# Performance work log

Measured on AMD Instinct MI355X. Metric: run time of the kernel, lower is better.

Reference implementation:

```python
import jax, jax.numpy as jnp
import numpy as np
import math

P = 2
TAU = 1.0
USE_POW = False
ALIGN_W = 1.0
ENTROPY_W = 1.0
EPS = 1e-12


def _pairwise_l2(z):
    # torch.cdist(z, z, p=2): sqrt of squared distances via GEMM decomposition
    sq = jnp.sum(z * z, axis=-1)  # [N]
    d2 = sq[:, None] + sq[None, :] - 2.0 * (z @ z.T)  # [N, N]
    d = jnp.sqrt(jnp.maximum(d2, 0.0))
    return jnp.maximum(d, EPS)  # clamp_min(eps)


def setup_inputs() -> dict:
    key = jax.random.key(0)
    k0, k1 = jax.random.split(key)
    v0 = jax.random.normal(k0, (8192, 256), dtype=jnp.float32)
    v1 = jax.random.normal(k1, (8192, 256), dtype=jnp.float32)
    return {"v0": v0, "v1": v1}


def reference(v0, v1):
    views = [v0, v1]
    n = v0.shape[0]

    # Alignment term: mean Lp distance between matched rows, one pair (0,1)
    diff = v0 - v1
    align = jnp.sqrt(jnp.sum(diff * diff, axis=-1)).mean()  # p=2 norm per row

    # Entropy term: masked logsumexp over within-view pairwise distances
    log_num_neg = math.log(n - 1)
    eye = jnp.eye(n, dtype=bool)
    entropy = jnp.float32(0.0)
    for z in views:
        dist = _pairwise_l2(z)  # [N, N]
        logits = jnp.where(eye, -jnp.inf, -dist / TAU)
        lme = jax.nn.logsumexp(logits, axis=1) - log_num_neg  # [N]
        entropy = entropy + lme.mean()
    entropy = entropy / len(views)

    return ALIGN_W * align + ENTROPY_W * entropy
```

## Files before the change

### kernel.cpp

```cpp
#include <hip/hip_runtime.h>
#include <math.h>


#define D_DIM 256
#define NB 64
#define NBLK 2080
#define S_Q 26.0f
#define LOG2E2 2.0813689810f
#define LP 65

typedef int i32x4 __attribute__((ext_vector_type(4)));
typedef unsigned int u32;
#define AS1 __attribute__((address_space(1)))
#define AS3 __attribute__((address_space(3)))

__device__ inline void load_lds16(const void* g, void* l) {
  __builtin_amdgcn_global_load_lds((const AS1 u32*)g, (AS3 u32*)l, 16, 0, 0);
}

__device__ inline int q8(float x) {
  return __float2int_rn(fminf(fmaxf(x * S_Q, -127.0f), 127.0f));
}
__device__ inline u32 q8x4(const float4 f) {
  return (u32)(q8(f.x) & 255) | ((u32)(q8(f.y) & 255) << 8) |
         ((u32)(q8(f.z) & 255) << 16) | ((u32)(q8(f.w) & 255) << 24);
}

__global__ __launch_bounds__(256) void prep(
    const float* __restrict__ v0, const float* __restrict__ v1,
    unsigned char* __restrict__ ph0, unsigned char* __restrict__ ph1,
    float* __restrict__ sq0, float* __restrict__ sq1,
    float* __restrict__ S0, float* __restrict__ S1,
    float* __restrict__ align_part) {
  __shared__ float4 l0[16 * LP], l1[16 * LP];
  __shared__ float red0[4][16], red1[4][16], red2[4][16];
  const int R = blockIdx.x;
  const int t = threadIdx.x;

  #pragma unroll
  for (int p = 0; p < 4; ++p) {
    const int slot = t + p * 256;
    const int r = slot >> 6, col = slot & 63;
    const size_t g = (size_t)(R * 16 + r) * 64 + col;
    l0[r * LP + col] = ((const float4*)v0)[g];
    l1[r * LP + col] = ((const float4*)v1)[g];
  }
  __syncthreads();

  {
    const int rr = t & 15, c = t >> 4;
    const int s = c >> 2, q = c & 3;
    const int li = rr * LP + c * 4;
    uint4 u0, u1;
    u0.x = q8x4(l0[li + 0]); u0.y = q8x4(l0[li + 1]);
    u0.z = q8x4(l0[li + 2]); u0.w = q8x4(l0[li + 3]);
    u1.x = q8x4(l1[li + 0]); u1.y = q8x4(l1[li + 1]);
    u1.z = q8x4(l1[li + 2]); u1.w = q8x4(l1[li + 3]);
    const size_t dst = (size_t)(R * 4 + s) * 64 + q * 16 + rr;
    ((uint4*)ph0)[dst] = u0;
    ((uint4*)ph1)[dst] = u1;
  }

  {
    const int rr = t & 15;
    const int base = rr * LP + (t >> 4) * 4;
    float s0p = 0.f, s1p = 0.f, s2p = 0.f;
    #pragma unroll
    for (int c = 0; c < 4; ++c) {
      const float4 a = l0[base + c], b = l1[base + c];
      s0p += a.x * a.x + a.y * a.y + a.z * a.z + a.w * a.w;
      s1p += b.x * b.x + b.y * b.y + b.z * b.z + b.w * b.w;
      const float dx = a.x - b.x, dy = a.y - b.y, dz = a.z - b.z, dw = a.w - b.w;
      s2p += dx * dx + dy * dy + dz * dz + dw * dw;
    }
    s0p += __shfl_xor(s0p, 16, 64); s0p += __shfl_xor(s0p, 32, 64);
    s1p += __shfl_xor(s1p, 16, 64); s1p += __shfl_xor(s1p, 32, 64);
    s2p += __shfl_xor(s2p, 16, 64); s2p += __shfl_xor(s2p, 32, 64);
    const int w = t >> 6, lane = t & 63;
    if (lane < 16) { red0[w][lane] = s0p; red1[w][lane] = s1p; red2[w][lane] = s2p; }
  }
  __syncthreads();
  if (t < 16) {
    const int row = R * 16 + t;
    const float a0 = red0[0][t] + red0[1][t] + red0[2][t] + red0[3][t];
    const float a1 = red1[0][t] + red1[1][t] + red1[2][t] + red1[3][t];
    const float a2 = red2[0][t] + red2[1][t] + red2[2][t] + red2[3][t];
    sq0[row] = a0 * LOG2E2;
    sq1[row] = a1 * LOG2E2;
    align_part[row] = sqrtf(a2);
    S0[row] = 0.0f;
    S1[row] = 0.0f;
  }
}

__global__ __launch_bounds__(256) void entropy_tile(
    const unsigned char* __restrict__ ph0, const unsigned char* __restrict__ ph1,
    const float* __restrict__ sq0, const float* __restrict__ sq1,
    float* __restrict__ S0, float* __restrict__ S1) {
  const int u = blockIdx.x;
  const int lin2 = (u & 7) * (2 * NBLK / 8) + (u >> 3);
  const int view = lin2 >= NBLK;
  const int lin = view ? lin2 - NBLK : lin2;

  const unsigned char* __restrict__ ph = view ? ph1 : ph0;
  const float* __restrict__ sq = view ? sq1 : sq0;
  float* __restrict__ S        = view ? S1 : S0;

  int bj = (int)((sqrt(8.0 * (double)lin + 1.0) - 1.0) * 0.5);
  while ((bj + 1) * (bj + 2) / 2 <= lin) ++bj;
  while (bj * (bj + 1) / 2 > lin) --bj;
  const int bi = lin - bj * (bj + 1) / 2;
  const bool diag = (bi == bj);

  __shared__ __align__(16) char smem[32768];
  float* swp = (float*)smem;

  const int t = threadIdx.x, lane = t & 63, w = t >> 6;
  const int wi = w >> 1, wj = w & 1;
  const int quad = lane >> 4, l15 = lane & 15;
  const int i0 = bi * 128, j0 = bj * 128;

  #pragma unroll
  for (int r8 = 0; r8 < 8; ++r8) {
    const int seg = w * 8 + r8;
    const unsigned char* src = ph + (size_t)bi * 32768 + seg * 1024 + lane * 16;
    load_lds16(src, smem + seg * 1024);
  }

  const i32x4* __restrict__ phv = (const i32x4*)ph;
  const int baseB = ((bj * 8 + wj * 4) * 4) * 64 + lane;

  i32x4 bF[2][4];
  #pragma unroll
  for (int n = 0; n < 4; ++n) bF[0][n] = phv[baseB + (n * 4) * 64];

  i32x4 acc[4][4];
  #pragma unroll
  for (int m = 0; m < 4; ++m)
    #pragma unroll
    for (int n = 0; n < 4; ++n)
      acc[m][n] = (i32x4){0, 0, 0, 0};

  float sj[4];
  #pragma unroll
  for (int n = 0; n < 4; ++n) sj[n] = sq[j0 + wj * 64 + n * 16 + l15];

  __syncthreads();

  const i32x4* smemv = (const i32x4*)smem;
  #pragma unroll
  for (int s = 0; s < 4; ++s) {
    const int cur = s & 1, nxt = cur ^ 1;
    if (s < 3) {
      #pragma unroll
      for (int n = 0; n < 4; ++n)
        bF[nxt][n] = phv[baseB + (n * 4 + s + 1) * 64];
    }
    i32x4 ah[4];
    #pragma unroll
    for (int m = 0; m < 4; ++m)
      ah[m] = smemv[(size_t)((wi * 4 + m) * 4 + s) * 64 + lane];
    #pragma unroll
    for (int m = 0; m < 4; ++m)
      #pragma unroll
      for (int n = 0; n < 4; ++n)
        acc[m][n] = __builtin_amdgcn_mfma_i32_16x16x64_i8(ah[m], bF[cur][n], acc[m][n], 0, 0, 0);
  }

  __syncthreads();

  const float K2 = 2.0f * LOG2E2 / (S_Q * S_Q);
  const int wbase = w * 1088;

  float csum[4] = {0.f, 0.f, 0.f, 0.f};
  #pragma unroll
  for (int m = 0; m < 4; ++m) {
    #pragma unroll
    for (int r = 0; r < 4; ++r) {
      const int rowl = m * 16 + quad * 4 + r;
      const int gi = i0 + wi * 64 + rowl;
      const float si = sq[gi];
      float p = 0.f;
      #pragma unroll
      for (int n = 0; n < 4; ++n) {
        const float d2 = fmaf(-K2, (float)acc[m][n][r], si + sj[n]);
        float e = __builtin_amdgcn_exp2f(-__builtin_amdgcn_sqrtf(d2));
        if (diag && gi == j0 + wj * 64 + n * 16 + l15) e = 0.f;
        p += e;
        csum[n] += e;
      }
      swp[wbase + rowl * 17 + l15] = p;
    }
  }
  {
    float rs = 0.f;
    #pragma unroll
    for (int j = 0; j < 16; ++j) rs += swp[wbase + lane * 17 + j];
    atomicAdd(&S[i0 + wi * 64 + lane], rs);
  }
  if (!diag) {
    #pragma unroll
    for (int n = 0; n < 4; ++n) {
      float c2 = csum[n];
      c2 += __shfl_xor(c2, 16, 64);
      c2 += __shfl_xor(c2, 32, 64);
      if (quad == 0) atomicAdd(&S[j0 + wj * 64 + n * 16 + l15], c2);
    }
  }
}

__global__ __launch_bounds__(256) void finalize_part(
    const float* __restrict__ S0, const float* __restrict__ S1,
    const float* __restrict__ align_part,
    float* __restrict__ part_log, float* __restrict__ part_align) {
  __shared__ float shl[4], sha[4];
  const int t = threadIdx.x, lane = t & 63, w = t >> 6;
  const int idx = blockIdx.x * 256 + t;
  float lg = __logf(S0[idx]) + __logf(S1[idx]);
  float al = align_part[idx];
  #pragma unroll
  for (int o = 1; o < 64; o <<= 1) {
    lg += __shfl_xor(lg, o, 64);
    al += __shfl_xor(al, o, 64);
  }
  if (lane == 0) { shl[w] = lg; sha[w] = al; }
  __syncthreads();
  if (t == 0) {
    part_log[blockIdx.x] = shl[0] + shl[1] + shl[2] + shl[3];
    part_align[blockIdx.x] = sha[0] + sha[1] + sha[2] + sha[3];
  }
}

__global__ void finalize_final(const float* __restrict__ part_log,
                               const float* __restrict__ part_align,
                               float* __restrict__ out, int n) {
  const int lane = threadIdx.x & 63;
  double lg = (lane < 32) ? (double)part_log[lane] : 0.0;
  double al = (lane < 32) ? (double)part_align[lane] : 0.0;
  #pragma unroll
  for (int o = 1; o < 32; o <<= 1) {
    lg += __shfl_xor(lg, o, 64);
    al += __shfl_xor(al, o, 64);
  }
  if (lane == 0) {
    double align = al / (double)n;
    double entropy = 0.5 * lg / (double)n - log((double)(n - 1));
    out[0] = (float)(align + entropy);
  }
}

extern "C" void kernel_launch(void* const* d_in, const int* in_sizes, int n_in,
                              void* d_out, int out_size, void* d_ws, size_t ws_size,
                              hipStream_t stream) {
  const float* v0 = (const float*)d_in[0];
  const float* v1 = (const float*)d_in[1];
  float* out = (float*)d_out;
  const int n = in_sizes[0] / D_DIM;

  float* ws         = (float*)d_ws;
  float* sq0        = ws;
  float* sq1        = ws + n;
  float* S0         = ws + 2 * n;
  float* S1         = ws + 3 * n;
  float* align_part = ws + 4 * n;
  float* part_log   = ws + 5 * n;
  float* part_align = ws + 5 * n + 32;
  unsigned char* ph0 = (unsigned char*)(ws + 5 * n + 64);
  unsigned char* ph1 = ph0 + (size_t)n * D_DIM;

  prep<<<n / 16, 256, 0, stream>>>(v0, v1, ph0, ph1, sq0, sq1, S0, S1, align_part);

  entropy_tile<<<2 * NBLK, 256, 0, stream>>>(ph0, ph1, sq0, sq1, S0, S1);

  finalize_part<<<n / 256, 256, 0, stream>>>(S0, S1, align_part, part_log, part_align);
  finalize_final<<<1, 64, 0, stream>>>(part_log, part_align, out, n);
}
```

Measured before the change: 121.9 us.

## Process two column tiles per block, reusing the LDS row panel and row sums

Each block now handles a pair of adjacent upper-triangular 128x128 tiles in the same block-row, so the A panel loaded into LDS and the per-row partial sums are shared across two tiles. This halves the row-sum atomics and the LDS panel loads, and cuts the grid from 4160 to 2112 blocks using a 2D grid (segments x view). The trade-offs are that the XCD-interleaving block remap is dropped and the row index is found with a linear search loop. Accumulators also stay live across both tiles, which raises register pressure.

New measurement: 112.2 us. 8.0% less time.

```diff
diff --git a/kernel.cpp b/kernel.cpp
--- a/kernel.cpp
+++ b/kernel.cpp
@@ -4,7 +4,7 @@
 
 #define D_DIM 256
 #define NB 64
-#define NBLK 2080
+#define NSEG 1056
 #define S_Q 26.0f
 #define LOG2E2 2.0813689810f
 #define LP 65
@@ -24,6 +24,11 @@
 __device__ inline u32 q8x4(const float4 f) {
   return (u32)(q8(f.x) & 255) | ((u32)(q8(f.y) & 255) << 8) |
          ((u32)(q8(f.z) & 255) << 16) | ((u32)(q8(f.w) & 255) << 24);
+}
+
+__device__ inline int Gfun(int M) {
+  const int m = M >> 1;
+  return (M & 1) ? (m + 1) * (m + 1) : m * (m + 1);
 }
 
 __global__ __launch_bounds__(256) void prep(
@@ -97,20 +102,15 @@
     const unsigned char* __restrict__ ph0, const unsigned char* __restrict__ ph1,
     const float* __restrict__ sq0, const float* __restrict__ sq1,
     float* __restrict__ S0, float* __restrict__ S1) {
-  const int u = blockIdx.x;
-  const int lin2 = (u & 7) * (2 * NBLK / 8) + (u >> 3);
-  const int view = lin2 >= NBLK;
-  const int lin = view ? lin2 - NBLK : lin2;
-
-  const unsigned char* __restrict__ ph = view ? ph1 : ph0;
-  const float* __restrict__ sq = view ? sq1 : sq0;
-  float* __restrict__ S        = view ? S1 : S0;
-
-  int bj = (int)((sqrt(8.0 * (double)lin + 1.0) - 1.0) * 0.5);
-  while ((bj + 1) * (bj + 2) / 2 <= lin) ++bj;
-  while (bj * (bj + 1) / 2 > lin) --bj;
-  const int bi = lin - bj * (bj + 1) / 2;
-  const bool diag = (bi == bj);
+  const unsigned char* __restrict__ ph = blockIdx.y ? ph1 : ph0;
+  const float* __restrict__ sq = blockIdx.y ? sq1 : sq0;
+  float* __restrict__ S        = blockIdx.y ? S1 : S0;
+
+  const int lin = blockIdx.x;
+  int bi = 0;
+  while (NSEG - Gfun(64 - (bi + 1)) <= lin) ++bi;
+  const int q = lin - (NSEG - Gfun(64 - bi));
+  const int bj0 = bi + 2 * q;
 
   __shared__ __align__(16) char smem[32768];
   float* swp = (float*)smem;
@@ -118,7 +118,7 @@
   const int t = threadIdx.x, lane = t & 63, w = t >> 6;
   const int wi = w >> 1, wj = w & 1;
   const int quad = lane >> 4, l15 = lane & 15;
-  const int i0 = bi * 128, j0 = bj * 128;
+  const int i0 = bi * 128;
 
   #pragma unroll
   for (int r8 = 0; r8 < 8; ++r8) {
@@ -126,87 +126,101 @@
     const unsigned char* src = ph + (size_t)bi * 32768 + seg * 1024 + lane * 16;
     load_lds16(src, smem + seg * 1024);
   }
+  __syncthreads();
 
   const i32x4* __restrict__ phv = (const i32x4*)ph;
-  const int baseB = ((bj * 8 + wj * 4) * 4) * 64 + lane;
-
-  i32x4 bF[2][4];
-  #pragma unroll
-  for (int n = 0; n < 4; ++n) bF[0][n] = phv[baseB + (n * 4) * 64];
-
-  i32x4 acc[4][4];
+  const i32x4* smemv = (const i32x4*)smem;
+  const float K2 = 2.0f * LOG2E2 / (S_Q * S_Q);
+
+  float prow[4][4];
   #pragma unroll
   for (int m = 0; m < 4; ++m)
     #pragma unroll
-    for (int n = 0; n < 4; ++n)
-      acc[m][n] = (i32x4){0, 0, 0, 0};
-
-  float sj[4];
-  #pragma unroll
-  for (int n = 0; n < 4; ++n) sj[n] = sq[j0 + wj * 64 + n * 16 + l15];
-
-  __syncthreads();
-
-  const i32x4* smemv = (const i32x4*)smem;
-  #pragma unroll
-  for (int s = 0; s < 4; ++s) {
-    const int cur = s & 1, nxt = cur ^ 1;
-    if (s < 3) {
-      #pragma unroll
-      for (int n = 0; n < 4; ++n)
-        bF[nxt][n] = phv[baseB + (n * 4 + s + 1) * 64];
-    }
-    i32x4 ah[4];
+    for (int r = 0; r < 4; ++r) prow[m][r] = 0.f;
+
+  auto do_tile = [&](const int bj, const bool diag_t) {
+    const int j0 = bj * 128;
+    const int baseB = ((bj * 8 + wj * 4) * 4) * 64 + lane;
+
+    float sjl[4];
+    #pragma unroll
+    for (int n = 0; n < 4; ++n) sjl[n] = sq[j0 + wj * 64 + n * 16 + l15];
+
+    i32x4 bF[2][4];
+    #pragma unroll
+    for (int n = 0; n < 4; ++n) bF[0][n] = phv[baseB + (n * 4) * 64];
+
+    i32x4 acc[4][4];
     #pragma unroll
     for (int m = 0; m < 4; ++m)
-      ah[m] = smemv[(size_t)((wi * 4 + m) * 4 + s) * 64 + lane];
-    #pragma unroll
-    for (int m = 0; m < 4; ++m)
-      #pragma unroll
-      for (int n = 0; n < 4; ++n)
-        acc[m][n] = __builtin_amdgcn_mfma_i32_16x16x64_i8(ah[m], bF[cur][n], acc[m][n], 0, 0, 0);
-  }
-
-  __syncthreads();
-
-  const float K2 = 2.0f * LOG2E2 / (S_Q * S_Q);
+      #pragma unroll
+      for (int n = 0; n < 4; ++n) acc[m][n] = (i32x4){0, 0, 0, 0};
+
+    #pragma unroll
+    for (int s = 0; s < 4; ++s) {
+      const int cur = s & 1, nxt = cur ^ 1;
+      if (s < 3) {
+        #pragma unroll
+        for (int n = 0; n < 4; ++n)
+          bF[nxt][n] = phv[baseB + (n * 4 + s + 1) * 64];
+      }
+      i32x4 ah[4];
+      #pragma unroll
+      for (int m = 0; m < 4; ++m)
+        ah[m] = smemv[(size_t)((wi * 4 + m) * 4 + s) * 64 + lane];
+      #pragma unroll
+      for (int m = 0; m < 4; ++m)
+        #pragma unroll
+        for (int n = 0; n < 4; ++n)
+          acc[m][n] = __builtin_amdgcn_mfma_i32_16x16x64_i8(ah[m], bF[cur][n], acc[m][n], 0, 0, 0);
+    }
+
+    float csum[4] = {0.f, 0.f, 0.f, 0.f};
+    #pragma unroll
+    for (int m = 0; m < 4; ++m) {
+      #pragma unroll
+      for (int r = 0; r < 4; ++r) {
+        const int rowl = m * 16 + quad * 4 + r;
+        const int gi = i0 + wi * 64 + rowl;
+        const float si = sq[gi];
+        float p = 0.f;
+        #pragma unroll
+        for (int n = 0; n < 4; ++n) {
+          const float d2 = fmaf(-K2, (float)acc[m][n][r], si + sjl[n]);
+          float e = __builtin_amdgcn_exp2f(-__builtin_amdgcn_sqrtf(d2));
+          if (diag_t && gi == j0 + wj * 64 + n * 16 + l15) e = 0.f;
+          p += e;
+          csum[n] += e;
+        }
+        prow[m][r] += p;
+      }
+    }
+    if (!diag_t) {
+      #pragma unroll
+      for (int n = 0; n < 4; ++n) {
+        float c2 = csum[n];
+        c2 += __shfl_xor(c2, 16, 64);
+        c2 += __shfl_xor(c2, 32, 64);
+        if (quad == 0) atomicAdd(&S[j0 + wj * 64 + n * 16 + l15], c2);
+      }
+    }
+  };
+
+  if (bj0 == bi) do_tile(bi, true); else do_tile(bj0, false);
+  if (bj0 + 1 < NB) do_tile(bj0 + 1, false);
+
+  __syncthreads();
+
   const int wbase = w * 1088;
-
-  float csum[4] = {0.f, 0.f, 0.f, 0.f};
-  #pragma unroll
-  for (int m = 0; m < 4; ++m) {
-    #pragma unroll
-    for (int r = 0; r < 4; ++r) {
-      const int rowl = m * 16 + quad * 4 + r;
-      const int gi = i0 + wi * 64 + rowl;
-      const float si = sq[gi];
-      float p = 0.f;
-      #pragma unroll
-      for (int n = 0; n < 4; ++n) {
-        const float d2 = fmaf(-K2, (float)acc[m][n][r], si + sj[n]);
-        float e = __builtin_amdgcn_exp2f(-__builtin_amdgcn_sqrtf(d2));
-        if (diag && gi == j0 + wj * 64 + n * 16 + l15) e = 0.f;
-        p += e;
-        csum[n] += e;
-      }
-      swp[wbase + rowl * 17 + l15] = p;
-    }
-  }
-  {
-    float rs = 0.f;
-    #pragma unroll
-    for (int j = 0; j < 16; ++j) rs += swp[wbase + lane * 17 + j];
-    atomicAdd(&S[i0 + wi * 64 + lane], rs);
-  }
-  if (!diag) {
-    #pragma unroll
-    for (int n = 0; n < 4; ++n) {
-      float c2 = csum[n];
-      c2 += __shfl_xor(c2, 16, 64);
-      c2 += __shfl_xor(c2, 32, 64);
-      if (quad == 0) atomicAdd(&S[j0 + wj * 64 + n * 16 + l15], c2);
-    }
-  }
+  #pragma unroll
+  for (int m = 0; m < 4; ++m)
+    #pragma unroll
+    for (int r = 0; r < 4; ++r)
+      swp[wbase + (m * 16 + quad * 4 + r) * 17 + l15] = prow[m][r];
+  float rs = 0.f;
+  #pragma unroll
+  for (int j = 0; j < 16; ++j) rs += swp[wbase + lane * 17 + j];
+  atomicAdd(&S[i0 + wi * 64 + lane], rs);
 }
 
 __global__ __launch_bounds__(256) void finalize_part(
@@ -270,7 +284,8 @@
 
   prep<<<n / 16, 256, 0, stream>>>(v0, v1, ph0, ph1, sq0, sq1, S0, S1, align_part);
 
-  entropy_tile<<<2 * NBLK, 256, 0, stream>>>(ph0, ph1, sq0, sq1, S0, S1);
+  dim3 grid(NSEG, 2);
+  entropy_tile<<<grid, 256, 0, stream>>>(ph0, ph1, sq0, sq1, S0, S1);
 
   finalize_part<<<n / 256, 256, 0, stream>>>(S0, S1, align_part, part_log, part_align);
   finalize_final<<<1, 64, 0, stream>>>(part_log, part_align, out, n);
```
